# Kernel optimization log

Hardware: AMD Instinct MI355X
Metric: run time of the kernel (lower is better)

The kernel has to match this reference:

```python
import jax, jax.numpy as jnp
import numpy as np

HIDDEN, MSG, KEY, ROUNDS = 256, 64, 16, 2
LN_EPS = 1e-5


def _orthogonal(key, shape, gain):
    # mimic torch orthogonal_ init (exact values don't matter for correctness testing)
    a = jax.random.normal(key, shape, dtype=jnp.float32)
    q, r = jnp.linalg.qr(a.T if shape[0] < shape[1] else a)
    q = q * jnp.sign(jnp.diag(r))
    if shape[0] < shape[1]:
        q = q.T
    return gain * q[:shape[0], :shape[1]]


def setup_inputs() -> dict:
    key = jax.random.key(0)
    ks = jax.random.split(key, 6)
    g = float(np.sqrt(2.0))
    N = 8192
    return {
        "hidden_states": jax.random.normal(ks[0], (N, HIDDEN), dtype=jnp.float32),
        "W_msg": _orthogonal(ks[1], (MSG, HIDDEN), g),
        "b_msg": jnp.zeros((MSG,), jnp.float32),
        "W_key": _orthogonal(ks[2], (KEY, HIDDEN), g),
        "b_key": jnp.zeros((KEY,), jnp.float32),
        "W_qry": _orthogonal(ks[3], (KEY, HIDDEN), g),
        "b_qry": jnp.zeros((KEY,), jnp.float32),
        "W_agg": _orthogonal(ks[4], (HIDDEN, HIDDEN + MSG), g),
        "b_agg": jnp.zeros((HIDDEN,), jnp.float32),
        "ln_g": jnp.ones((HIDDEN,), jnp.float32),
        "ln_b": jnp.zeros((HIDDEN,), jnp.float32),
    }


def reference(hidden_states, W_msg, b_msg, W_key, b_key, W_qry, b_qry,
              W_agg, b_agg, ln_g, ln_b):
    inv_sqrt_k = 1.0 / np.sqrt(KEY)
    h = hidden_states
    attn = None
    for _ in range(ROUNDS):
        msgs = h @ W_msg.T + b_msg          # (N, MSG)
        keys = h @ W_key.T + b_key          # (N, KEY)
        qrys = h @ W_qry.T + b_qry          # (N, KEY)
        scores = (qrys @ keys.T) * inv_sqrt_k  # (N, N)
        attn = jax.nn.softmax(scores, axis=-1)
        agg_msg = attn @ msgs               # (N, MSG)
        combined = jnp.concatenate([h, agg_msg], axis=-1)  # (N, HIDDEN+MSG)
        z = combined @ W_agg.T + b_agg      # (N, HIDDEN)
        mu = jnp.mean(z, axis=-1, keepdims=True)
        var = jnp.mean(jnp.square(z - mu), axis=-1, keepdims=True)
        h = jax.nn.relu(ln_g * (z - mu) * jax.lax.rsqrt(var + LN_EPS) + ln_b)
    return h, attn
```

## Files before the change

kernel.cpp:

```cpp
#include <hip/hip_runtime.h>

constexpr int H = 256, MSGC = 64;
constexpr float LN_EPS = 1e-5f;
constexpr float QSCALE = 0.25f * 1.4426950408889634f;

typedef __attribute__((ext_vector_type(8))) short bf16x8;
typedef __attribute__((ext_vector_type(4))) float f32x4;

__device__ inline ushort f2bf(float x) {
    union { float f; unsigned u; } v; v.f = x;
    unsigned r = v.u + 0x7fffu + ((v.u >> 16) & 1u);
    return (ushort)(r >> 16);
}
__device__ inline float bf2f(ushort h) {
    union { unsigned u; float f; } v; v.u = ((unsigned)h) << 16;
    return v.f;
}
__device__ inline bf16x8 pack_bf16x8(float4 f0, float4 f1) {
    union { unsigned u[4]; bf16x8 v; } cv;
    asm("v_cvt_pk_bf16_f32 %0, %1, %2" : "=v"(cv.u[0]) : "v"(f0.x), "v"(f0.y));
    asm("v_cvt_pk_bf16_f32 %0, %1, %2" : "=v"(cv.u[1]) : "v"(f0.z), "v"(f0.w));
    asm("v_cvt_pk_bf16_f32 %0, %1, %2" : "=v"(cv.u[2]) : "v"(f1.x), "v"(f1.y));
    asm("v_cvt_pk_bf16_f32 %0, %1, %2" : "=v"(cv.u[3]) : "v"(f1.z), "v"(f1.w));
    return cv.v;
}

__global__ __launch_bounds__(256) void prep_kernel(
    const float* __restrict__ Wm, const float* __restrict__ Wk,
    const float* __restrict__ Wq, const float* __restrict__ Wa,
    ushort* __restrict__ Wph, ushort* __restrict__ Wpl,
    ushort* __restrict__ Wfh, ushort* __restrict__ Wfl)
{
    const int t = threadIdx.x, b = blockIdx.x;
    if (b < 48) {
        const int tile = b >> 3, kc = b & 7;
#pragma unroll
        for (int j2 = 0; j2 < 2; ++j2) {
            const int idx = t * 2 + j2;
            const int l = idx >> 3, e = idx & 7;
            const int col = tile * 16 + (l & 15);
            const int k = kc * 32 + (l >> 4) * 8 + e;
            float v;
            if (col < 64)      v = Wm[(size_t)col * H + k];
            else if (col < 80) v = Wk[(size_t)(col - 64) * H + k];
            else               v = QSCALE * Wq[(size_t)(col - 80) * H + k];
            ushort hi = f2bf(v);
            Wph[(size_t)b * 512 + idx] = hi;
            Wpl[(size_t)b * 512 + idx] = f2bf(v - bf2f(hi));
        }
    } else {
        const int unit = b - 48;
        const int ctg = unit / 10, kc = unit % 10;
#pragma unroll
        for (int j2 = 0; j2 < 2; ++j2) {
            const int idx = t * 2 + j2;
            const int l = idx >> 3, e = idx & 7;
            const int col = ctg * 16 + (l & 15);
            const int k = kc * 32 + (l >> 4) * 8 + e;
            const float v = Wa[(size_t)col * 320 + k];
            ushort hi = f2bf(v);
            Wfh[(size_t)unit * 512 + idx] = hi;
            Wfl[(size_t)unit * 512 + idx] = f2bf(v - bf2f(hi));
        }
    }
}

__global__ __launch_bounds__(128) void proj_kernel(
    const float* __restrict__ h,
    const ushort* __restrict__ Wph, const ushort* __restrict__ Wpl,
    const float* __restrict__ bm, const float* __restrict__ bk, const float* __restrict__ bq,
    ushort* __restrict__ msgsF, ushort* __restrict__ kh, ushort* __restrict__ kl,
    ushort* __restrict__ qh, ushort* __restrict__ ql, int n)
{
    constexpr int AST = 264;
    __shared__ ushort Ahi[16 * AST];
    __shared__ ushort Alo[16 * AST];
    const int t = threadIdx.x, lane = t & 63, w = t >> 6;
    const int gq = lane >> 4, c = lane & 15;
    const int r0 = blockIdx.x * 16;
    const float4* hsrc = (const float4*)(h + (size_t)r0 * H);
#pragma unroll
    for (int u = 0; u < 8; ++u) {
        const int idx = t + 128 * u;
        const int row = idx >> 6, c4 = idx & 63;
        float4 v = hsrc[idx];
        ushort4 hi, lo;
        hi.x = f2bf(v.x); lo.x = f2bf(v.x - bf2f(hi.x));
        hi.y = f2bf(v.y); lo.y = f2bf(v.y - bf2f(hi.y));
        hi.z = f2bf(v.z); lo.z = f2bf(v.z - bf2f(hi.z));
        hi.w = f2bf(v.w); lo.w = f2bf(v.w - bf2f(hi.w));
        *(ushort4*)&Ahi[row * AST + c4 * 4] = hi;
        *(ushort4*)&Alo[row * AST + c4 * 4] = lo;
    }
    __syncthreads();
    f32x4 acc[3] = {{0,0,0,0},{0,0,0,0},{0,0,0,0}};
    for (int kc = 0; kc < 8; ++kc) {
        const bf16x8 afh = *(const bf16x8*)&Ahi[c * AST + kc * 32 + gq * 8];
        const bf16x8 afl = *(const bf16x8*)&Alo[c * AST + kc * 32 + gq * 8];
#pragma unroll
        for (int ct = 0; ct < 3; ++ct) {
            const int unit = (w * 3 + ct) * 8 + kc;
            const bf16x8 whi = *(const bf16x8*)(Wph + (size_t)unit * 512 + lane * 8);
            const bf16x8 wlo = *(const bf16x8*)(Wpl + (size_t)unit * 512 + lane * 8);
            acc[ct] = __builtin_amdgcn_mfma_f32_16x16x32_bf16(afh, whi, acc[ct], 0, 0, 0);
            acc[ct] = __builtin_amdgcn_mfma_f32_16x16x32_bf16(afh, wlo, acc[ct], 0, 0, 0);
            acc[ct] = __builtin_amdgcn_mfma_f32_16x16x32_bf16(afl, whi, acc[ct], 0, 0, 0);
        }
    }
#pragma unroll
    for (int ct = 0; ct < 3; ++ct) {
        const int tile = w * 3 + ct;
        if (tile < 4) {
            const float bb = bm[tile * 16 + c];
#pragma unroll
            for (int r = 0; r < 4; ++r) {
                const int j = r0 + gq * 4 + r;
                const size_t idx = ((size_t)(j >> 5) * 4 + tile) * 512
                                 + ((j >> 3) & 3) * 128 + c * 8 + (j & 7);
                msgsF[idx] = f2bf(acc[ct][r] + bb);
            }
        } else if (tile == 4) {
            const float bb = bk[c];
#pragma unroll
            for (int r = 0; r < 4; ++r) {
                const int j = r0 + gq * 4 + r;
                const float v = acc[ct][r] + bb;
                const ushort hi = f2bf(v);
                kh[(size_t)j * 16 + c] = hi;
                kl[(size_t)j * 16 + c] = f2bf(v - bf2f(hi));
            }
        } else {
            const float bb = QSCALE * bq[c];
#pragma unroll
            for (int r = 0; r < 4; ++r) {
                const int j = r0 + gq * 4 + r;
                const float v = acc[ct][r] + bb;
                const ushort hi = f2bf(v);
                qh[(size_t)j * 16 + c] = hi;
                ql[(size_t)j * 16 + c] = f2bf(v - bf2f(hi));
            }
        }
    }
}

__device__ __forceinline__ void loadK(bf16x8* dst, const ushort* __restrict__ kh,
                                      int j0, int g, int c) {
#pragma unroll
    for (int js = 0; js < 4; ++js)
        dst[js] = *(const bf16x8*)(kh + (size_t)(j0 + js * 16 + c) * 16 + 8 * (g & 1));
}

__device__ __forceinline__ void qk_tile(const bf16x8* b1s, const ushort* __restrict__ kl,
                                        int j0, int g, int c, bf16x8 a1, bf16x8 a2,
                                        const bf16x8 zer, f32x4* pd) {
    const f32x4 z4 = {0.f, 0.f, 0.f, 0.f};
    bf16x8 b2s[4];
#pragma unroll
    for (int js = 0; js < 4; ++js)
        b2s[js] = (g < 2) ? *(const bf16x8*)(kl + (size_t)(j0 + js * 16 + c) * 16 + 8 * g) : zer;
#pragma unroll
    for (int js = 0; js < 4; ++js) {
        pd[js] = __builtin_amdgcn_mfma_f32_16x16x32_bf16(a1, b1s[js], z4, 0, 0, 0);
        pd[js] = __builtin_amdgcn_mfma_f32_16x16x32_bf16(a2, b2s[js], pd[js], 0, 0, 0);
    }
}

__device__ __forceinline__ void pv_tile(const float* __restrict__ P,
                                        const ushort* __restrict__ msgsF,
                                        int j0, int g, int c, int w, int lane, f32x4* accv) {
#pragma unroll
    for (int ks = 0; ks < 2; ++ks) {
        const int arow = w * 16 + c;
        const int sw = (arow & 7) << 2;
        const int colb = ks * 32 + 8 * g;
        float4 f0 = *(const float4*)&P[arow * 64 + ((colb) ^ sw)];
        float4 f1 = *(const float4*)&P[arow * 64 + ((colb + 4) ^ sw)];
        bf16x8 af = pack_bf16x8(f0, f1);
        const size_t mbase = ((size_t)(j0 >> 5) + ks) * 4;
#pragma unroll
        for (int mt = 0; mt < 4; ++mt) {
            bf16x8 bfr = *((const bf16x8*)(msgsF + (mbase + mt) * 512) + lane);
            accv[mt] = __builtin_amdgcn_mfma_f32_16x16x32_bf16(af, bfr, accv[mt], 0, 0, 0);
        }
    }
}

__device__ __forceinline__ void expstore(const f32x4* pd, float* Pbuf, float* l,
                                         int w, int g, int c) {
#pragma unroll
    for (int js = 0; js < 4; ++js)
#pragma unroll
        for (int r = 0; r < 4; ++r) {
            const int row = w * 16 + g * 4 + r;
            const float pp = exp2f(pd[js][r]);
            l[r] += pp;
            Pbuf[row * 64 + ((js * 16 + c) ^ ((row & 7) << 2))] = pp;
        }
}

__device__ __forceinline__ void expstore_n(const f32x4* pd, float* Pbuf, const float* rinv,
                                           int w, int g, int c) {
#pragma unroll
    for (int js = 0; js < 4; ++js)
#pragma unroll
        for (int r = 0; r < 4; ++r) {
            const int row = w * 16 + g * 4 + r;
            const float pp = exp2f(pd[js][r]) * rinv[r];
            Pbuf[row * 64 + ((js * 16 + c) ^ ((row & 7) << 2))] = pp;
        }
}

__device__ __forceinline__ void attn_write(const float* __restrict__ Pbuf,
                                           float* __restrict__ attn,
                                           int i0, int j0, int n, int lane, int w) {
    const int c4 = lane & 15;
#pragma unroll
    for (int u = 0; u < 4; ++u) {
        const int row = w * 16 + u * 4 + (lane >> 4);
        const int sw = (row & 7) << 2;
        float4 v = *(const float4*)&Pbuf[row * 64 + ((c4 * 4) ^ sw)];
        *(float4*)(attn + (size_t)(i0 + row) * n + j0 + c4 * 4) = v;
    }
}

__global__ __launch_bounds__(256, 4) void flash1_kernel(
    const ushort* __restrict__ qh, const ushort* __restrict__ ql,
    const ushort* __restrict__ kh, const ushort* __restrict__ kl,
    const ushort* __restrict__ msgsF,
    float* __restrict__ aggO, float* __restrict__ aggL, int n)
{
    __shared__ float P0[64 * 64];
    __shared__ float P1[64 * 64];
    const int t = threadIdx.x, lane = t & 63, w = t >> 6;
    const int g = lane >> 4, c = lane & 15;
    const int i0 = blockIdx.x * 64;
    bf16x8 zer = {0,0,0,0,0,0,0,0};
    f32x4 z4 = {0.f, 0.f, 0.f, 0.f};
    const ushort* qsrc = (g < 2) ? qh : ql;
    bf16x8 a1 = *(const bf16x8*)(qsrc + (size_t)(i0 + w * 16 + c) * 16 + 8 * (g & 1));
    bf16x8 a2 = (g < 2) ? a1 : zer;
    float l[4] = {0.f, 0.f, 0.f, 0.f};
    f32x4 accv[4] = {z4, z4, z4, z4};
    const int nj = n / 8, jb = blockIdx.y * nj;
    bf16x8 bA[4], bB[4];
    loadK(bA, kh, jb, g, c);
    loadK(bB, kh, jb + 64, g, c);
    {
        f32x4 pd[4];
        qk_tile(bA, kl, jb, g, c, a1, a2, zer, pd);
        expstore(pd, P0, l, w, g, c);
    }
    loadK(bA, kh, jb + 128, g, c);
    {
        f32x4 pd[4];
        qk_tile(bB, kl, jb + 64, g, c, a1, a2, zer, pd);
        pv_tile(P0, msgsF, jb, g, c, w, lane, accv);
        expstore(pd, P1, l, w, g, c);
    }
    for (int p = 1; p < 8; ++p) {
        const int tA = jb + p * 128, tB = tA + 64;
        loadK(bB, kh, tB, g, c);
        {
            f32x4 pd[4];
            qk_tile(bA, kl, tA, g, c, a1, a2, zer, pd);
            pv_tile(P1, msgsF, tA - 64, g, c, w, lane, accv);
            expstore(pd, P0, l, w, g, c);
        }
        loadK(bA, kh, (p < 7) ? tA + 128 : tB, g, c);
        {
            f32x4 pd[4];
            qk_tile(bB, kl, tB, g, c, a1, a2, zer, pd);
            pv_tile(P0, msgsF, tA, g, c, w, lane, accv);
            expstore(pd, P1, l, w, g, c);
        }
    }
    pv_tile(P1, msgsF, jb + nj - 64, g, c, w, lane, accv);
#pragma unroll
    for (int r = 0; r < 4; ++r)
#pragma unroll
        for (int d2 = 1; d2 < 16; d2 <<= 1) l[r] += __shfl_xor(l[r], d2, 64);
#pragma unroll
    for (int mt = 0; mt < 4; ++mt)
#pragma unroll
        for (int r = 0; r < 4; ++r)
            aggO[((size_t)blockIdx.y * n + i0 + w * 16 + g * 4 + r) * MSGC + mt * 16 + c] = accv[mt][r];
    if (c == 0) {
#pragma unroll
        for (int r = 0; r < 4; ++r)
            aggL[(size_t)blockIdx.y * n + i0 + w * 16 + g * 4 + r] = l[r];
    }
}

__global__ __launch_bounds__(256, 4) void stats_kernel(
    const ushort* __restrict__ qh, const ushort* __restrict__ ql,
    const ushort* __restrict__ kh, const ushort* __restrict__ kl,
    float* __restrict__ rowl_p, int n)
{
    const int t = threadIdx.x, lane = t & 63, w = t >> 6;
    const int g = lane >> 4, c = lane & 15;
    const int iq = blockIdx.x * 64 + w * 16 + c;
    bf16x8 zer = {0,0,0,0,0,0,0,0};
    const ushort* qsrc = (g < 2) ? qh : ql;
    bf16x8 a1 = *(const bf16x8*)(qsrc + (size_t)iq * 16 + 8 * (g & 1));
    bf16x8 a2 = (g < 2) ? a1 : zer;
    const int nj = n / 8, jb = blockIdx.y * nj;
    float l[4] = {0.f, 0.f, 0.f, 0.f};
    bf16x8 bA[4], bB[4];
    loadK(bA, kh, jb, g, c);
    for (int p = 0; p < 8; ++p) {
        const int t0 = jb + p * 128, t1 = t0 + 64;
        const int t2 = (p < 7) ? t0 + 128 : t1;
        loadK(bB, kh, t1, g, c);
        {
            f32x4 pd[4];
            qk_tile(bA, kl, t0, g, c, a1, a2, zer, pd);
#pragma unroll
            for (int js = 0; js < 4; ++js)
#pragma unroll
                for (int r = 0; r < 4; ++r) l[r] += exp2f(pd[js][r]);
        }
        loadK(bA, kh, t2, g, c);
        {
            f32x4 pd[4];
            qk_tile(bB, kl, t1, g, c, a1, a2, zer, pd);
#pragma unroll
            for (int js = 0; js < 4; ++js)
#pragma unroll
                for (int r = 0; r < 4; ++r) l[r] += exp2f(pd[js][r]);
        }
    }
#pragma unroll
    for (int r = 0; r < 4; ++r)
#pragma unroll
        for (int d2 = 1; d2 < 16; d2 <<= 1) l[r] += __shfl_xor(l[r], d2, 64);
    if (c == 0) {
        const int q0 = blockIdx.x * 64 + w * 16 + g * 4;
#pragma unroll
        for (int r = 0; r < 4; ++r)
            rowl_p[(size_t)blockIdx.y * n + q0 + r] = l[r];
    }
}

__global__ __launch_bounds__(256, 4) void pass2_kernel(
    const ushort* __restrict__ qh, const ushort* __restrict__ ql,
    const ushort* __restrict__ kh, const ushort* __restrict__ kl,
    const ushort* __restrict__ msgsF, const float* __restrict__ rowl_p,
    float* __restrict__ aggO, float* __restrict__ attn, int n)
{
    __shared__ float P0[64 * 64];
    __shared__ float P1[64 * 64];
    const int t = threadIdx.x, lane = t & 63, w = t >> 6;
    const int g = lane >> 4, c = lane & 15;
    const int i0 = blockIdx.x * 64;
    bf16x8 zer = {0,0,0,0,0,0,0,0};
    f32x4 z4 = {0.f, 0.f, 0.f, 0.f};
    const ushort* qsrc = (g < 2) ? qh : ql;
    bf16x8 a1 = *(const bf16x8*)(qsrc + (size_t)(i0 + w * 16 + c) * 16 + 8 * (g & 1));
    bf16x8 a2 = (g < 2) ? a1 : zer;
    float rinv[4];
#pragma unroll
    for (int r = 0; r < 4; ++r) {
        const int q = i0 + w * 16 + g * 4 + r;
        float L = 0.f;
#pragma unroll
        for (int p = 0; p < 8; ++p) L += rowl_p[(size_t)p * n + q];
        rinv[r] = 1.f / L;
    }
    f32x4 accv[4] = {z4, z4, z4, z4};
    const int nj = n / 8, jb = blockIdx.y * nj;
    bf16x8 bA[4], bB[4];
    loadK(bA, kh, jb, g, c);
    loadK(bB, kh, jb + 64, g, c);
    {
        f32x4 pd[4];
        qk_tile(bA, kl, jb, g, c, a1, a2, zer, pd);
        expstore_n(pd, P0, rinv, w, g, c);
    }
    loadK(bA, kh, jb + 128, g, c);
    {
        f32x4 pd[4];
        qk_tile(bB, kl, jb + 64, g, c, a1, a2, zer, pd);
        attn_write(P0, attn, i0, jb, n, lane, w);
        pv_tile(P0, msgsF, jb, g, c, w, lane, accv);
        expstore_n(pd, P1, rinv, w, g, c);
    }
    for (int p = 1; p < 8; ++p) {
        const int tA = jb + p * 128, tB = tA + 64;
        loadK(bB, kh, tB, g, c);
        {
            f32x4 pd[4];
            qk_tile(bA, kl, tA, g, c, a1, a2, zer, pd);
            attn_write(P1, attn, i0, tA - 64, n, lane, w);
            pv_tile(P1, msgsF, tA - 64, g, c, w, lane, accv);
            expstore_n(pd, P0, rinv, w, g, c);
        }
        loadK(bA, kh, (p < 7) ? tA + 128 : tB, g, c);
        {
            f32x4 pd[4];
            qk_tile(bB, kl, tB, g, c, a1, a2, zer, pd);
            attn_write(P0, attn, i0, tA, n, lane, w);
            pv_tile(P0, msgsF, tA, g, c, w, lane, accv);
            expstore_n(pd, P1, rinv, w, g, c);
        }
    }
    attn_write(P1, attn, i0, jb + nj - 64, n, lane, w);
    pv_tile(P1, msgsF, jb + nj - 64, g, c, w, lane, accv);
#pragma unroll
    for (int mt = 0; mt < 4; ++mt)
#pragma unroll
        for (int r = 0; r < 4; ++r) {
            const int row = w * 16 + g * 4 + r;
            aggO[((size_t)blockIdx.y * n + i0 + row) * MSGC + mt * 16 + c] = accv[mt][r];
        }
}

template <bool FLASH>
__global__ __launch_bounds__(256) void aggln_kernel(
    const float* __restrict__ h, const float* __restrict__ aggO,
    const float* __restrict__ aggL,
    const ushort* __restrict__ Wfh, const ushort* __restrict__ Wfl,
    const float* __restrict__ ba,
    const float* __restrict__ gg, const float* __restrict__ bb,
    float* __restrict__ hout, int n)
{
    constexpr int AST = 328;
    __shared__ ushort Ahi[16 * AST];
    __shared__ ushort Alo[16 * AST];
    __shared__ float Linv[16];
    __shared__ float red1[16][4], red2[16][4];
    const int t = threadIdx.x, lane = t & 63, w = t >> 6;
    const int gq = lane >> 4, c = lane & 15;
    const int r0 = blockIdx.x * 16;
    const float4* hsrc = (const float4*)(h + (size_t)r0 * H);
#pragma unroll
    for (int u = 0; u < 4; ++u) {
        const int idx = t + 256 * u;
        const int row = idx >> 6, c4 = idx & 63;
        float4 v = hsrc[idx];
        ushort4 hi, lo;
        hi.x = f2bf(v.x); lo.x = f2bf(v.x - bf2f(hi.x));
        hi.y = f2bf(v.y); lo.y = f2bf(v.y - bf2f(hi.y));
        hi.z = f2bf(v.z); lo.z = f2bf(v.z - bf2f(hi.z));
        hi.w = f2bf(v.w); lo.w = f2bf(v.w - bf2f(hi.w));
        *(ushort4*)&Ahi[row * AST + c4 * 4] = hi;
        *(ushort4*)&Alo[row * AST + c4 * 4] = lo;
    }
    if (FLASH && t < 16) {
        float L = 0.f;
#pragma unroll
        for (int p = 0; p < 8; ++p) L += aggL[(size_t)p * n + r0 + t];
        Linv[t] = 1.f / L;
    }
    __syncthreads();
    {
        const int row = t >> 4, c4 = t & 15;
        float4 s = {0.f, 0.f, 0.f, 0.f};
#pragma unroll
        for (int p = 0; p < 8; ++p) {
            const float4 v = *(const float4*)(aggO + (size_t)p * n * MSGC
                               + (size_t)(r0 + row) * MSGC + c4 * 4);
            s.x += v.x; s.y += v.y; s.z += v.z; s.w += v.w;
        }
        if (FLASH) { const float li = Linv[row]; s.x *= li; s.y *= li; s.z *= li; s.w *= li; }
        ushort4 hi, lo;
        hi.x = f2bf(s.x); lo.x = f2bf(s.x - bf2f(hi.x));
        hi.y = f2bf(s.y); lo.y = f2bf(s.y - bf2f(hi.y));
        hi.z = f2bf(s.z); lo.z = f2bf(s.z - bf2f(hi.z));
        hi.w = f2bf(s.w); lo.w = f2bf(s.w - bf2f(hi.w));
        *(ushort4*)&Ahi[row * AST + 256 + c4 * 4] = hi;
        *(ushort4*)&Alo[row * AST + 256 + c4 * 4] = lo;
    }
    __syncthreads();
    f32x4 acc[4] = {{0,0,0,0},{0,0,0,0},{0,0,0,0},{0,0,0,0}};
    for (int kc = 0; kc < 10; ++kc) {
        const bf16x8 afh = *(const bf16x8*)&Ahi[c * AST + kc * 32 + gq * 8];
        const bf16x8 afl = *(const bf16x8*)&Alo[c * AST + kc * 32 + gq * 8];
#pragma unroll
        for (int ct = 0; ct < 4; ++ct) {
            const int ctg = w * 4 + ct;
            const bf16x8 whi = *(const bf16x8*)(Wfh + ((size_t)(ctg * 10 + kc)) * 512 + lane * 8);
            const bf16x8 wlo = *(const bf16x8*)(Wfl + ((size_t)(ctg * 10 + kc)) * 512 + lane * 8);
            acc[ct] = __builtin_amdgcn_mfma_f32_16x16x32_bf16(afh, whi, acc[ct], 0, 0, 0);
            acc[ct] = __builtin_amdgcn_mfma_f32_16x16x32_bf16(afh, wlo, acc[ct], 0, 0, 0);
            acc[ct] = __builtin_amdgcn_mfma_f32_16x16x32_bf16(afl, whi, acc[ct], 0, 0, 0);
        }
    }
    float bav[4], gv[4], bv[4];
#pragma unroll
    for (int ct = 0; ct < 4; ++ct) {
        const int col = w * 64 + ct * 16 + c;
        bav[ct] = ba[col]; gv[ct] = gg[col]; bv[ct] = bb[col];
    }
#pragma unroll
    for (int ct = 0; ct < 4; ++ct) {
        acc[ct][0] += bav[ct]; acc[ct][1] += bav[ct];
        acc[ct][2] += bav[ct]; acc[ct][3] += bav[ct];
    }
#pragma unroll
    for (int r = 0; r < 4; ++r) {
        float s1 = 0.f, s2 = 0.f;
#pragma unroll
        for (int ct = 0; ct < 4; ++ct) { const float v = acc[ct][r]; s1 += v; s2 += v * v; }
#pragma unroll
        for (int d = 1; d < 16; d <<= 1) { s1 += __shfl_xor(s1, d, 64); s2 += __shfl_xor(s2, d, 64); }
        if (c == 0) { red1[gq * 4 + r][w] = s1; red2[gq * 4 + r][w] = s2; }
    }
    __syncthreads();
#pragma unroll
    for (int r = 0; r < 4; ++r) {
        const int row = gq * 4 + r;
        const float s1 = red1[row][0] + red1[row][1] + red1[row][2] + red1[row][3];
        const float s2 = red2[row][0] + red2[row][1] + red2[row][2] + red2[row][3];
        const float mu = s1 * (1.f / 256.f);
        const float var = s2 * (1.f / 256.f) - mu * mu;
        const float rs = rsqrtf(var + LN_EPS);
#pragma unroll
        for (int ct = 0; ct < 4; ++ct) {
            float o = (acc[ct][r] - mu) * rs * gv[ct] + bv[ct];
            hout[(size_t)(r0 + row) * H + w * 64 + ct * 16 + c] = fmaxf(o, 0.f);
        }
    }
}

extern "C" void kernel_launch(void* const* d_in, const int* in_sizes, int n_in,
                              void* d_out, int out_size, void* d_ws, size_t ws_size,
                              hipStream_t stream)
{
    const float* hs = (const float*)d_in[0];
    const float* Wm = (const float*)d_in[1];
    const float* bm = (const float*)d_in[2];
    const float* Wk = (const float*)d_in[3];
    const float* bk = (const float*)d_in[4];
    const float* Wq = (const float*)d_in[5];
    const float* bq = (const float*)d_in[6];
    const float* Wa = (const float*)d_in[7];
    const float* ba = (const float*)d_in[8];
    const float* lg = (const float*)d_in[9];
    const float* lb = (const float*)d_in[10];
    const int n = in_sizes[0] / H;

    char* wp = (char*)d_ws;
    auto alloc = [&](size_t bytes) { void* p = (void*)wp; wp += (bytes + 255) & ~(size_t)255; return p; };
    float*  h2     = (float*)alloc((size_t)n * H * 4);
    ushort* qh     = (ushort*)alloc((size_t)n * 16 * 2);
    ushort* ql     = (ushort*)alloc((size_t)n * 16 * 2);
    ushort* kh     = (ushort*)alloc((size_t)n * 16 * 2);
    ushort* kl     = (ushort*)alloc((size_t)n * 16 * 2);
    ushort* msgsF  = (ushort*)alloc((size_t)MSGC * n * 2);
    float*  rowl_p = (float*)alloc((size_t)8 * n * 4);
    float*  aggO   = (float*)alloc((size_t)8 * n * MSGC * 4);
    float*  aggL   = (float*)alloc((size_t)8 * n * 4);
    ushort* Wph    = (ushort*)alloc((size_t)48 * 512 * 2);
    ushort* Wpl    = (ushort*)alloc((size_t)48 * 512 * 2);
    ushort* Wfh    = (ushort*)alloc((size_t)160 * 512 * 2);
    ushort* Wfl    = (ushort*)alloc((size_t)160 * 512 * 2);

    float* hOut = (float*)d_out;
    float* attn = hOut + (size_t)n * H;

    prep_kernel<<<208, 256, 0, stream>>>(Wm, Wk, Wq, Wa, Wph, Wpl, Wfh, Wfl);

    proj_kernel<<<n / 16, 128, 0, stream>>>(hs, Wph, Wpl, bm, bk, bq, msgsF, kh, kl, qh, ql, n);
    flash1_kernel<<<dim3(n / 64, 8), 256, 0, stream>>>(qh, ql, kh, kl, msgsF,
                                                       aggO, aggL, n);
    aggln_kernel<true><<<n / 16, 256, 0, stream>>>(hs, aggO, aggL, Wfh, Wfl,
                                                   ba, lg, lb, h2, n);
    proj_kernel<<<n / 16, 128, 0, stream>>>(h2, Wph, Wpl, bm, bk, bq, msgsF, kh, kl, qh, ql, n);
    stats_kernel<<<dim3(n / 64, 8), 256, 0, stream>>>(qh, ql, kh, kl, rowl_p, n);
    pass2_kernel<<<dim3(n / 64, 8), 256, 0, stream>>>(qh, ql, kh, kl, msgsF,
                                                      rowl_p, aggO, attn, n);
    aggln_kernel<false><<<n / 16, 256, 0, stream>>>(h2, aggO, aggL, Wfh, Wfl,
                                                    ba, lg, lb, hOut, n);
}
```

Measured before the change: 244.5 us.

## Store softmax probabilities as packed bf16 in LDS with permuted msgs layout

The P tile in shared memory changes from fp32 to bf16. Probabilities are packed with v_cvt_pk_bf16_f32 at exp time, and the PV MFMA A-fragment is read with a single 16-byte LDS load instead of two float4 loads plus conversion. The msgs fragment layout is permuted so that the column pairing matches the new packed P layout. This halves LDS footprint and traffic and removes per-tile conversion. The trade-offs are that the attn output is now written from bf16-rounded values, which loses precision, and attn global stores become scalar rather than float4.

```diff
diff --git a/kernel.cpp b/kernel.cpp
--- a/kernel.cpp
+++ b/kernel.cpp
@@ -16,13 +16,10 @@
     union { unsigned u; float f; } v; v.u = ((unsigned)h) << 16;
     return v.f;
 }
-__device__ inline bf16x8 pack_bf16x8(float4 f0, float4 f1) {
-    union { unsigned u[4]; bf16x8 v; } cv;
-    asm("v_cvt_pk_bf16_f32 %0, %1, %2" : "=v"(cv.u[0]) : "v"(f0.x), "v"(f0.y));
-    asm("v_cvt_pk_bf16_f32 %0, %1, %2" : "=v"(cv.u[1]) : "v"(f0.z), "v"(f0.w));
-    asm("v_cvt_pk_bf16_f32 %0, %1, %2" : "=v"(cv.u[2]) : "v"(f1.x), "v"(f1.y));
-    asm("v_cvt_pk_bf16_f32 %0, %1, %2" : "=v"(cv.u[3]) : "v"(f1.z), "v"(f1.w));
-    return cv.v;
+__device__ inline unsigned cvt_pk_u32(float a, float b) {
+    unsigned r;
+    asm("v_cvt_pk_bf16_f32 %0, %1, %2" : "=v"(r) : "v"(a), "v"(b));
+    return r;
 }
 
 __global__ __launch_bounds__(256) void prep_kernel(
@@ -115,8 +112,10 @@
 #pragma unroll
             for (int r = 0; r < 4; ++r) {
                 const int j = r0 + gq * 4 + r;
+                const int o = j & 31;
+                const int lam = ((o & 15) << 1) | (o >> 4);
                 const size_t idx = ((size_t)(j >> 5) * 4 + tile) * 512
-                                 + ((j >> 3) & 3) * 128 + c * 8 + (j & 7);
+                                 + (lam >> 3) * 128 + c * 8 + (lam & 7);
                 msgsF[idx] = f2bf(acc[ct][r] + bb);
             }
         } else if (tile == 4) {
@@ -165,18 +164,45 @@
     }
 }
 
-__device__ __forceinline__ void pv_tile(const float* __restrict__ P,
-                                        const ushort* __restrict__ msgsF,
-                                        int j0, int g, int c, int w, int lane, f32x4* accv) {
-#pragma unroll
-    for (int ks = 0; ks < 2; ++ks) {
-        const int arow = w * 16 + c;
-        const int sw = (arow & 7) << 2;
-        const int colb = ks * 32 + 8 * g;
-        float4 f0 = *(const float4*)&P[arow * 64 + ((colb) ^ sw)];
-        float4 f1 = *(const float4*)&P[arow * 64 + ((colb + 4) ^ sw)];
-        bf16x8 af = pack_bf16x8(f0, f1);
-        const size_t mbase = ((size_t)(j0 >> 5) + ks) * 4;
+__device__ __forceinline__ void expstore_bf(const f32x4* pd, ushort* Pbuf, float* l,
+                                            int w, int g, int c) {
+#pragma unroll
+    for (int r = 0; r < 4; ++r) {
+        const int row = w * 16 + g * 4 + r;
+        const float e0 = exp2f(pd[0][r]);
+        const float e1 = exp2f(pd[1][r]);
+        const float e2 = exp2f(pd[2][r]);
+        const float e3 = exp2f(pd[3][r]);
+        l[r] += (e0 + e1) + (e2 + e3);
+        ushort* base = Pbuf + row * 64;
+        *(unsigned*)&base[(((c >> 2)) ^ (row & 7)) * 8 + (c & 3) * 2]     = cvt_pk_u32(e0, e1);
+        *(unsigned*)&base[((4 + (c >> 2)) ^ (row & 7)) * 8 + (c & 3) * 2] = cvt_pk_u32(e2, e3);
+    }
+}
+__device__ __forceinline__ void expstore_n_bf(const f32x4* pd, ushort* Pbuf, const float* rinv,
+                                              int w, int g, int c) {
+#pragma unroll
+    for (int r = 0; r < 4; ++r) {
+        const int row = w * 16 + g * 4 + r;
+        const float e0 = exp2f(pd[0][r]) * rinv[r];
+        const float e1 = exp2f(pd[1][r]) * rinv[r];
+        const float e2 = exp2f(pd[2][r]) * rinv[r];
+        const float e3 = exp2f(pd[3][r]) * rinv[r];
+        ushort* base = Pbuf + row * 64;
+        *(unsigned*)&base[(((c >> 2)) ^ (row & 7)) * 8 + (c & 3) * 2]     = cvt_pk_u32(e0, e1);
+        *(unsigned*)&base[((4 + (c >> 2)) ^ (row & 7)) * 8 + (c & 3) * 2] = cvt_pk_u32(e2, e3);
+    }
+}
+
+__device__ __forceinline__ void pv_bf(const ushort* __restrict__ Pbuf,
+                                      const ushort* __restrict__ msgsF,
+                                      int j0, int g, int c, int w, int lane, f32x4* accv) {
+    const int arow = w * 16 + c;
+    const int sw = arow & 7;
+#pragma unroll
+    for (int gam = 0; gam < 2; ++gam) {
+        const bf16x8 af = *(const bf16x8*)&Pbuf[arow * 64 + ((gam * 4 + g) ^ sw) * 8];
+        const size_t mbase = ((size_t)(j0 >> 5) + gam) * 4;
 #pragma unroll
         for (int mt = 0; mt < 4; ++mt) {
             bf16x8 bfr = *((const bf16x8*)(msgsF + (mbase + mt) * 512) + lane);
@@ -185,41 +211,22 @@
     }
 }
 
-__device__ __forceinline__ void expstore(const f32x4* pd, float* Pbuf, float* l,
-                                         int w, int g, int c) {
-#pragma unroll
-    for (int js = 0; js < 4; ++js)
-#pragma unroll
-        for (int r = 0; r < 4; ++r) {
-            const int row = w * 16 + g * 4 + r;
-            const float pp = exp2f(pd[js][r]);
-            l[r] += pp;
-            Pbuf[row * 64 + ((js * 16 + c) ^ ((row & 7) << 2))] = pp;
-        }
-}
-
-__device__ __forceinline__ void expstore_n(const f32x4* pd, float* Pbuf, const float* rinv,
-                                           int w, int g, int c) {
-#pragma unroll
-    for (int js = 0; js < 4; ++js)
-#pragma unroll
-        for (int r = 0; r < 4; ++r) {
-            const int row = w * 16 + g * 4 + r;
-            const float pp = exp2f(pd[js][r]) * rinv[r];
-            Pbuf[row * 64 + ((js * 16 + c) ^ ((row & 7) << 2))] = pp;
-        }
-}
-
-__device__ __forceinline__ void attn_write(const float* __restrict__ Pbuf,
-                                           float* __restrict__ attn,
-                                           int i0, int j0, int n, int lane, int w) {
-    const int c4 = lane & 15;
+__device__ __forceinline__ void attn_write_bf(const ushort* __restrict__ Pbuf,
+                                              float* __restrict__ attn,
+                                              int i0, int j0, int n, int lane, int w) {
+    const int g4 = lane >> 4, c4 = lane & 15;
 #pragma unroll
     for (int u = 0; u < 4; ++u) {
-        const int row = w * 16 + u * 4 + (lane >> 4);
-        const int sw = (row & 7) << 2;
-        float4 v = *(const float4*)&Pbuf[row * 64 + ((c4 * 4) ^ sw)];
-        *(float4*)(attn + (size_t)(i0 + row) * n + j0 + c4 * 4) = v;
+        const int row = w * 16 + u * 4 + g4;
+        const int sw = row & 7;
+        const ushort* base = Pbuf + row * 64;
+        float* arow = attn + (size_t)(i0 + row) * n + j0;
+#pragma unroll
+        for (int gam = 0; gam < 2; ++gam) {
+            const unsigned uv = *(const unsigned*)&base[((gam * 4 + (c4 >> 2)) ^ sw) * 8 + (c4 & 3) * 2];
+            arow[gam * 32 + c4]      = bf2f((ushort)(uv & 0xffffu));
+            arow[gam * 32 + c4 + 16] = bf2f((ushort)(uv >> 16));
+        }
     }
 }
 
@@ -229,8 +236,8 @@
     const ushort* __restrict__ msgsF,
     float* __restrict__ aggO, float* __restrict__ aggL, int n)
 {
-    __shared__ float P0[64 * 64];
-    __shared__ float P1[64 * 64];
+    __shared__ ushort P0[64 * 64];
+    __shared__ ushort P1[64 * 64];
     const int t = threadIdx.x, lane = t & 63, w = t >> 6;
     const int g = lane >> 4, c = lane & 15;
     const int i0 = blockIdx.x * 64;
@@ -248,14 +255,14 @@
     {
         f32x4 pd[4];
         qk_tile(bA, kl, jb, g, c, a1, a2, zer, pd);
-        expstore(pd, P0, l, w, g, c);
+        expstore_bf(pd, P0, l, w, g, c);
     }
     loadK(bA, kh, jb + 128, g, c);
     {
         f32x4 pd[4];
         qk_tile(bB, kl, jb + 64, g, c, a1, a2, zer, pd);
-        pv_tile(P0, msgsF, jb, g, c, w, lane, accv);
-        expstore(pd, P1, l, w, g, c);
+        pv_bf(P0, msgsF, jb, g, c, w, lane, accv);
+        expstore_bf(pd, P1, l, w, g, c);
     }
     for (int p = 1; p < 8; ++p) {
         const int tA = jb + p * 128, tB = tA + 64;
@@ -263,18 +270,18 @@
         {
             f32x4 pd[4];
             qk_tile(bA, kl, tA, g, c, a1, a2, zer, pd);
-            pv_tile(P1, msgsF, tA - 64, g, c, w, lane, accv);
-            expstore(pd, P0, l, w, g, c);
+            pv_bf(P1, msgsF, tA - 64, g, c, w, lane, accv);
+            expstore_bf(pd, P0, l, w, g, c);
         }
         loadK(bA, kh, (p < 7) ? tA + 128 : tB, g, c);
         {
             f32x4 pd[4];
             qk_tile(bB, kl, tB, g, c, a1, a2, zer, pd);
-            pv_tile(P0, msgsF, tA, g, c, w, lane, accv);
-            expstore(pd, P1, l, w, g, c);
-        }
-    }
-    pv_tile(P1, msgsF, jb + nj - 64, g, c, w, lane, accv);
+            pv_bf(P0, msgsF, tA, g, c, w, lane, accv);
+            expstore_bf(pd, P1, l, w, g, c);
+        }
+    }
+    pv_bf(P1, msgsF, jb + nj - 64, g, c, w, lane, accv);
 #pragma unroll
     for (int r = 0; r < 4; ++r)
 #pragma unroll
@@ -347,8 +354,8 @@
     const ushort* __restrict__ msgsF, const float* __restrict__ rowl_p,
     float* __restrict__ aggO, float* __restrict__ attn, int n)
 {
-    __shared__ float P0[64 * 64];
-    __shared__ float P1[64 * 64];
+    __shared__ ushort P0[64 * 64];
+    __shared__ ushort P1[64 * 64];
     const int t = threadIdx.x, lane = t & 63, w = t >> 6;
     const int g = lane >> 4, c = lane & 15;
     const int i0 = blockIdx.x * 64;
@@ -374,15 +381,15 @@
     {
         f32x4 pd[4];
         qk_tile(bA, kl, jb, g, c, a1, a2, zer, pd);
-        expstore_n(pd, P0, rinv, w, g, c);
+        expstore_n_bf(pd, P0, rinv, w, g, c);
     }
     loadK(bA, kh, jb + 128, g, c);
     {
         f32x4 pd[4];
         qk_tile(bB, kl, jb + 64, g, c, a1, a2, zer, pd);
-        attn_write(P0, attn, i0, jb, n, lane, w);
-        pv_tile(P0, msgsF, jb, g, c, w, lane, accv);
-        expstore_n(pd, P1, rinv, w, g, c);
+        pv_bf(P0, msgsF, jb, g, c, w, lane, accv);
+        attn_write_bf(P0, attn, i0, jb, n, lane, w);
+        expstore_n_bf(pd, P1, rinv, w, g, c);
     }
     for (int p = 1; p < 8; ++p) {
         const int tA = jb + p * 128, tB = tA + 64;
@@ -390,21 +397,21 @@
         {
             f32x4 pd[4];
             qk_tile(bA, kl, tA, g, c, a1, a2, zer, pd);
-            attn_write(P1, attn, i0, tA - 64, n, lane, w);
-            pv_tile(P1, msgsF, tA - 64, g, c, w, lane, accv);
-            expstore_n(pd, P0, rinv, w, g, c);
+            pv_bf(P1, msgsF, tA - 64, g, c, w, lane, accv);
+            attn_write_bf(P1, attn, i0, tA - 64, n, lane, w);
+            expstore_n_bf(pd, P0, rinv, w, g, c);
         }
         loadK(bA, kh, (p < 7) ? tA + 128 : tB, g, c);
         {
             f32x4 pd[4];
             qk_tile(bB, kl, tB, g, c, a1, a2, zer, pd);
-            attn_write(P0, attn, i0, tA, n, lane, w);
-            pv_tile(P0, msgsF, tA, g, c, w, lane, accv);
-            expstore_n(pd, P1, rinv, w, g, c);
-        }
-    }
-    attn_write(P1, attn, i0, jb + nj - 64, n, lane, w);
-    pv_tile(P1, msgsF, jb + nj - 64, g, c, w, lane, accv);
+            pv_bf(P0, msgsF, tA, g, c, w, lane, accv);
+            attn_write_bf(P0, attn, i0, tA, n, lane, w);
+            expstore_n_bf(pd, P1, rinv, w, g, c);
+        }
+    }
+    pv_bf(P1, msgsF, jb + nj - 64, g, c, w, lane, accv);
+    attn_write_bf(P1, attn, i0, jb + nj - 64, n, lane, w);
 #pragma unroll
     for (int mt = 0; mt < 4; ++mt)
 #pragma unroll
```

Measured after the change: 255.8 us. +4.6%, slower.
